# Kernel optimization log

Hardware: AMD Instinct MI355X
Metric: run time of the kernel (lower is better)

Reference implementation:

```python
import jax, jax.numpy as jnp
import numpy as np

BATCH, NODES, HIDDEN = 64, 207, 64
DT = 0.01
STEPS = 100  # integrate t from 0 to 1 with Euler-Maruyama


def _gcn(y3, A, W, b):
    # y3: [B, N, H] -> tanh(A @ Y @ W + b)
    return jnp.tanh(jnp.einsum('mn,bnh->bmh', A, y3) @ W + b)


def setup_inputs() -> dict:
    key = jax.random.key(0)
    ks = jax.random.split(key, 8)
    scale = 1.0 / np.sqrt(HIDDEN)
    x = jax.random.normal(ks[0], (BATCH, NODES, HIDDEN), dtype=jnp.float32)
    A = jax.random.uniform(ks[1], (NODES, NODES), dtype=jnp.float32)
    A = A / A.sum(axis=-1, keepdims=True)  # row-normalized adjacency
    W_trend = scale * jax.random.normal(ks[2], (HIDDEN, HIDDEN), dtype=jnp.float32)
    b_trend = jnp.zeros((HIDDEN,), dtype=jnp.float32)
    W_diff = scale * jax.random.normal(ks[3], (HIDDEN, HIDDEN), dtype=jnp.float32)
    b_diff = jnp.zeros((HIDDEN,), dtype=jnp.float32)
    W_out = scale * jax.random.normal(ks[4], (HIDDEN, HIDDEN * HIDDEN), dtype=jnp.float32)
    b_out = jnp.zeros((HIDDEN * HIDDEN,), dtype=jnp.float32)
    return {"x": x, "A": A, "W_trend": W_trend, "b_trend": b_trend,
            "W_diff": W_diff, "b_diff": b_diff, "W_out": W_out, "b_out": b_out}


def reference(x, A, W_trend, b_trend, W_diff, b_diff, W_out, b_out):
    B = x.shape[0]
    y0 = x.reshape(B, -1)  # [B, N*H]
    noise_keys = jax.random.split(jax.random.key(42), STEPS)
    sqrt_dt = jnp.sqrt(jnp.asarray(DT, dtype=y0.dtype))
    dt = jnp.asarray(DT, dtype=y0.dtype)

    def step(y, k):
        y3 = y.reshape(B, NODES, HIDDEN)
        # Abstract_SDE scales both drift and diffusion by 0.1
        F = 0.1 * _gcn(y3, A, W_trend, b_trend).reshape(B, -1)
        G = 0.1 * _gcn(y3, A, W_diff, b_diff).reshape(B, -1)
        dW = sqrt_dt * jax.random.normal(k, y.shape, dtype=y.dtype)
        return y + F * dt + G * dW, None

    yT, _ = jax.lax.scan(step, y0, noise_keys)
    z = yT.reshape(B, NODES, HIDDEN)
    z = z @ W_out + b_out  # [B, N, H*H]
    return jnp.tanh(z.reshape(B, NODES, HIDDEN, HIDDEN))
```

## Files before the change

kernel.cpp:

```cpp
#include <hip/hip_runtime.h>
#include <cstdint>

#define BATCH 64
#define NODES 207
#define HID   64
#define NH    (NODES*HID)
#define TOT   (BATCH*NH)
#define NSTEPS 100
#define MT 28
#define NT 8
#define ASTR 208

__device__ __forceinline__ uint32_t rotl32(uint32_t v, int n) {
    return (v << n) | (v >> (32 - n));
}

__device__ __forceinline__ void threefry2x32(uint32_t k0, uint32_t k1,
                                             uint32_t& x0, uint32_t& x1) {
    uint32_t ks0 = k0, ks1 = k1, ks2 = k0 ^ k1 ^ 0x1BD11BDAu;
    x0 += ks0; x1 += ks1;
#define TF_ROUND(r) { x0 += x1; x1 = rotl32(x1, (r)); x1 ^= x0; }
    TF_ROUND(13) TF_ROUND(15) TF_ROUND(26) TF_ROUND(6)
    x0 += ks1; x1 += ks2 + 1u;
    TF_ROUND(17) TF_ROUND(29) TF_ROUND(16) TF_ROUND(24)
    x0 += ks2; x1 += ks0 + 2u;
    TF_ROUND(13) TF_ROUND(15) TF_ROUND(26) TF_ROUND(6)
    x0 += ks0; x1 += ks1 + 3u;
    TF_ROUND(17) TF_ROUND(29) TF_ROUND(16) TF_ROUND(24)
    x0 += ks1; x1 += ks2 + 4u;
    TF_ROUND(13) TF_ROUND(15) TF_ROUND(26) TF_ROUND(6)
    x0 += ks2; x1 += ks0 + 5u;
#undef TF_ROUND
}

__device__ __forceinline__ float erfinv32(float x) {
    float w = -log1pf(-x * x);
    float p;
    if (w < 5.0f) {
        w = w - 2.5f;
        p =             2.81022636e-08f;
        p = fmaf(p, w,  3.43273939e-07f);
        p = fmaf(p, w, -3.5233877e-06f);
        p = fmaf(p, w, -4.39150654e-06f);
        p = fmaf(p, w,  0.00021858087f);
        p = fmaf(p, w, -0.00125372503f);
        p = fmaf(p, w, -0.00417768164f);
        p = fmaf(p, w,  0.246640727f);
        p = fmaf(p, w,  1.50140941f);
    } else {
        w = sqrtf(w) - 3.0f;
        p =            -0.000200214257f;
        p = fmaf(p, w,  0.000100950558f);
        p = fmaf(p, w,  0.00134934322f);
        p = fmaf(p, w, -0.00367342844f);
        p = fmaf(p, w,  0.00573950773f);
        p = fmaf(p, w, -0.0076224613f);
        p = fmaf(p, w,  0.00943887047f);
        p = fmaf(p, w,  1.00167406f);
        p = fmaf(p, w,  2.83297682f);
    }
    return p * x;
}

__device__ __forceinline__ float bits_to_normal(uint32_t bits) {
    uint32_t fb = (bits >> 9) | 0x3f800000u;
    float f = __uint_as_float(fb) - 1.0f;
    const float lo = -0.99999994f;
    float u = f * 2.0f + lo;
    u = fmaxf(lo, u);
    return 1.41421356237f * erfinv32(u);
}


__global__ void k_init(const float* __restrict__ x, float* __restrict__ y,
                       uint32_t* __restrict__ keys) {
    int tid = blockIdx.x * blockDim.x + threadIdx.x;
    int n4 = TOT / 4;
    int stride = gridDim.x * blockDim.x;
    for (int i = tid; i < n4; i += stride) {
        ((float4*)y)[i] = ((const float4*)x)[i];
    }
    if (tid < NSTEPS) {
        uint32_t x0 = 0u, x1 = (uint32_t)tid;
        threefry2x32(0u, 42u, x0, x1);
        keys[2*tid]   = x0;
        keys[2*tid+1] = x1;
    }
}

__global__ __launch_bounds__(512) void k_fused(const float* __restrict__ A,
                                               const float* __restrict__ yin,
                                               float* __restrict__ yout,
                                               const float* __restrict__ Wt,
                                               const float* __restrict__ bt,
                                               const float* __restrict__ Wd,
                                               const float* __restrict__ bd,
                                               const uint32_t* __restrict__ keys,
                                               int s) {
    __shared__ __align__(16) float Alds[MT * ASTR];
    __shared__ __align__(16) float AYs[MT * HID];
    int b  = blockIdx.x;
    int m0 = blockIdx.y * MT;
    int h  = threadIdx.x & 63;
    int r  = __builtin_amdgcn_readfirstlane((int)(threadIdx.x >> 6));

    for (int row = r; row < MT; row += 8) {
        int m = m0 + row;
        const float* src = A + (size_t)m * NODES;
        bool v = (m < NODES);
        for (int c = h; c < NODES; c += 64)
            Alds[row*ASTR + c] = v ? src[c] : 0.0f;
    }
    __syncthreads();

    int rl[4];
#pragma unroll
    for (int i = 0; i < 4; ++i) {
        int t = r + 8*i;
        rl[i] = (t < MT) ? t : (MT - 1);
    }

    const float* yb = yin + (size_t)b * NH;
    float acc[4] = {0.f, 0.f, 0.f, 0.f};
#pragma unroll 2
    for (int n = 0; n < 204; n += 4) {
        float y0 = yb[(n+0)*HID + h];
        float y1 = yb[(n+1)*HID + h];
        float y2 = yb[(n+2)*HID + h];
        float y3 = yb[(n+3)*HID + h];
#pragma unroll
        for (int i = 0; i < 4; ++i) {
            float4 a4 = *(const float4*)&Alds[rl[i]*ASTR + n];
            acc[i] = fmaf(a4.x, y0, acc[i]);
            acc[i] = fmaf(a4.y, y1, acc[i]);
            acc[i] = fmaf(a4.z, y2, acc[i]);
            acc[i] = fmaf(a4.w, y3, acc[i]);
        }
    }
#pragma unroll 1
    for (int n = 204; n < NODES; ++n) {
        float yv = yb[n*HID + h];
#pragma unroll
        for (int i = 0; i < 4; ++i)
            acc[i] = fmaf(Alds[rl[i]*ASTR + n], yv, acc[i]);
    }

#pragma unroll
    for (int i = 0; i < 4; ++i) {
        int t = r + 8*i;
        if (t < MT) AYs[t*HID + h] = acc[i];
    }

    float accT[4] = {0.f, 0.f, 0.f, 0.f};
    float accD[4] = {0.f, 0.f, 0.f, 0.f};
#pragma unroll 2
    for (int k = 0; k < HID; k += 4) {
        float wt0 = Wt[(k+0)*HID + h], wt1 = Wt[(k+1)*HID + h];
        float wt2 = Wt[(k+2)*HID + h], wt3 = Wt[(k+3)*HID + h];
        float wd0 = Wd[(k+0)*HID + h], wd1 = Wd[(k+1)*HID + h];
        float wd2 = Wd[(k+2)*HID + h], wd3 = Wd[(k+3)*HID + h];
#pragma unroll
        for (int i = 0; i < 4; ++i) {
            float4 a4 = *(const float4*)&AYs[rl[i]*HID + k];
            accT[i] = fmaf(a4.x, wt0, accT[i]);
            accT[i] = fmaf(a4.y, wt1, accT[i]);
            accT[i] = fmaf(a4.z, wt2, accT[i]);
            accT[i] = fmaf(a4.w, wt3, accT[i]);
            accD[i] = fmaf(a4.x, wd0, accD[i]);
            accD[i] = fmaf(a4.y, wd1, accD[i]);
            accD[i] = fmaf(a4.z, wd2, accD[i]);
            accD[i] = fmaf(a4.w, wd3, accD[i]);
        }
    }

    uint32_t kk0 = keys[2*s], kk1 = keys[2*s+1];
    float btv = bt[h], bdv = bd[h];
#pragma unroll
    for (int i = 0; i < 4; ++i) {
        int t = r + 8*i;
        int m = m0 + t;
        if (t < MT && m < NODES) {
            float F = 0.1f * tanhf(accT[i] + btv);
            float G = 0.1f * tanhf(accD[i] + bdv);
            uint32_t j = (uint32_t)(((size_t)b*NODES + m)*HID + h);
            uint32_t x0 = 0u, x1 = j;
            threefry2x32(kk0, kk1, x0, x1);
            float nrm = bits_to_normal(x0 ^ x1);
            float dW  = 0.1f * nrm;
            float yold = yb[(size_t)m*HID + h];
            yout[(size_t)b*NH + (size_t)m*HID + h] = (yold + F * 0.01f) + G * dW;
        }
    }
}

#define OR 16
__global__ __launch_bounds__(256) void k_out(const float* __restrict__ y,
                                             const float* __restrict__ Wo,
                                             const float* __restrict__ bo,
                                             float* __restrict__ out) {
    int r0   = blockIdx.x * OR;
    int col0 = blockIdx.y * 1024 + threadIdx.x * 4;
    const float* yb = y + (size_t)r0 * HID;
    float4 acc[OR];
#pragma unroll
    for (int r = 0; r < OR; ++r) acc[r] = make_float4(0.f, 0.f, 0.f, 0.f);
#pragma unroll 4
    for (int k = 0; k < HID; ++k) {
        float4 wv = *(const float4*)&Wo[(size_t)k*4096 + col0];
#pragma unroll
        for (int r = 0; r < OR; ++r) {
            float yv = yb[r*HID + k];
            acc[r].x = fmaf(yv, wv.x, acc[r].x);
            acc[r].y = fmaf(yv, wv.y, acc[r].y);
            acc[r].z = fmaf(yv, wv.z, acc[r].z);
            acc[r].w = fmaf(yv, wv.w, acc[r].w);
        }
    }
    float4 bb = *(const float4*)&bo[col0];
#pragma unroll
    for (int r = 0; r < OR; ++r) {
        float4 o;
        o.x = tanhf(acc[r].x + bb.x);
        o.y = tanhf(acc[r].y + bb.y);
        o.z = tanhf(acc[r].z + bb.z);
        o.w = tanhf(acc[r].w + bb.w);
        *(float4*)&out[(size_t)(r0 + r)*4096 + col0] = o;
    }
}

extern "C" void kernel_launch(void* const* d_in, const int* in_sizes, int n_in,
                              void* d_out, int out_size, void* d_ws, size_t ws_size,
                              hipStream_t stream) {
    const float* x  = (const float*)d_in[0];
    const float* A  = (const float*)d_in[1];
    const float* Wt = (const float*)d_in[2];
    const float* bt = (const float*)d_in[3];
    const float* Wd = (const float*)d_in[4];
    const float* bd = (const float*)d_in[5];
    const float* Wo = (const float*)d_in[6];
    const float* bo = (const float*)d_in[7];
    float* out = (float*)d_out;

    float* y0 = (float*)d_ws;
    float* y1 = y0 + TOT;
    uint32_t* keys = (uint32_t*)(y1 + TOT);

    k_init<<<512, 256, 0, stream>>>(x, y0, keys);
    float* cur = y0;
    float* nxt = y1;
    for (int s = 0; s < NSTEPS; ++s) {
        k_fused<<<dim3(BATCH, NT), 512, 0, stream>>>(A, cur, nxt, Wt, bt, Wd, bd, keys, s);
        float* t = cur; cur = nxt; nxt = t;
    }
    k_out<<<dim3(NH/OR, 4096/1024), 256, 0, stream>>>(cur, Wo, bo, out);
}
```

Measured before the change: 2.707 ms.

## Replace per-step launches with persistent kernel using per-batch global barriers

The 100 per-step kernel launches become one persistent kernel of 512 blocks. Blocks for the same batch sync through a per-batch atomic counter barrier, and the A tile stays in LDS across all steps. The step keys are now computed per block in LDS. This removes launch overhead and the repeated A reload, but it depends on all 512 blocks being co-resident (launch_bounds 512,2) and adds spin-wait cost at every step. After 100 steps the final state lands in y0, which is what k_out reads.

After: 5.764 ms. 2.13x slower.

```diff
diff --git a/kernel.cpp b/kernel.cpp
--- a/kernel.cpp
+++ b/kernel.cpp
@@ -73,36 +73,33 @@
 
 
 __global__ void k_init(const float* __restrict__ x, float* __restrict__ y,
-                       uint32_t* __restrict__ keys) {
+                       uint32_t* __restrict__ bar) {
     int tid = blockIdx.x * blockDim.x + threadIdx.x;
     int n4 = TOT / 4;
     int stride = gridDim.x * blockDim.x;
     for (int i = tid; i < n4; i += stride) {
         ((float4*)y)[i] = ((const float4*)x)[i];
     }
-    if (tid < NSTEPS) {
-        uint32_t x0 = 0u, x1 = (uint32_t)tid;
-        threefry2x32(0u, 42u, x0, x1);
-        keys[2*tid]   = x0;
-        keys[2*tid+1] = x1;
-    }
-}
-
-__global__ __launch_bounds__(512) void k_fused(const float* __restrict__ A,
-                                               const float* __restrict__ yin,
-                                               float* __restrict__ yout,
-                                               const float* __restrict__ Wt,
-                                               const float* __restrict__ bt,
-                                               const float* __restrict__ Wd,
-                                               const float* __restrict__ bd,
-                                               const uint32_t* __restrict__ keys,
-                                               int s) {
+    if (tid < 1024) bar[tid] = 0u;
+}
+
+__global__ __launch_bounds__(512, 2) void k_persist(const float* __restrict__ A,
+                                                    float* y0g,
+                                                    float* y1g,
+                                                    const float* __restrict__ Wt,
+                                                    const float* __restrict__ bt,
+                                                    const float* __restrict__ Wd,
+                                                    const float* __restrict__ bd,
+                                                    uint32_t* bar) {
     __shared__ __align__(16) float Alds[MT * ASTR];
     __shared__ __align__(16) float AYs[MT * HID];
-    int b  = blockIdx.x;
-    int m0 = blockIdx.y * MT;
-    int h  = threadIdx.x & 63;
-    int r  = __builtin_amdgcn_readfirstlane((int)(threadIdx.x >> 6));
+    __shared__ uint32_t Klds[2 * NSTEPS];
+    int bid = blockIdx.x;
+    int b   = bid >> 3;
+    int t8  = bid & 7;
+    int m0  = t8 * MT;
+    int h   = threadIdx.x & 63;
+    int r   = __builtin_amdgcn_readfirstlane((int)(threadIdx.x >> 6));
 
     for (int row = r; row < MT; row += 8) {
         int m = m0 + row;
@@ -111,6 +108,12 @@
         for (int c = h; c < NODES; c += 64)
             Alds[row*ASTR + c] = v ? src[c] : 0.0f;
     }
+    if (threadIdx.x < NSTEPS) {
+        uint32_t x0 = 0u, x1 = (uint32_t)threadIdx.x;
+        threefry2x32(0u, 42u, x0, x1);
+        Klds[2*threadIdx.x]   = x0;
+        Klds[2*threadIdx.x+1] = x1;
+    }
     __syncthreads();
 
     int rl[4];
@@ -120,76 +123,99 @@
         rl[i] = (t < MT) ? t : (MT - 1);
     }
 
-    const float* yb = yin + (size_t)b * NH;
-    float acc[4] = {0.f, 0.f, 0.f, 0.f};
+    float* cur = y0g;
+    float* nxt = y1g;
+    uint32_t* mybar = bar + b * 16;
+
+#pragma unroll 1
+    for (int s = 0; s < NSTEPS; ++s) {
+        const float* yb = cur + (size_t)b * NH;
+
+        float acc[4] = {0.f, 0.f, 0.f, 0.f};
 #pragma unroll 2
-    for (int n = 0; n < 204; n += 4) {
-        float y0 = yb[(n+0)*HID + h];
-        float y1 = yb[(n+1)*HID + h];
-        float y2 = yb[(n+2)*HID + h];
-        float y3 = yb[(n+3)*HID + h];
+        for (int n = 0; n < 204; n += 4) {
+            float y0 = yb[(n+0)*HID + h];
+            float y1 = yb[(n+1)*HID + h];
+            float y2 = yb[(n+2)*HID + h];
+            float y3 = yb[(n+3)*HID + h];
+#pragma unroll
+            for (int i = 0; i < 4; ++i) {
+                float4 a4 = *(const float4*)&Alds[rl[i]*ASTR + n];
+                acc[i] = fmaf(a4.x, y0, acc[i]);
+                acc[i] = fmaf(a4.y, y1, acc[i]);
+                acc[i] = fmaf(a4.z, y2, acc[i]);
+                acc[i] = fmaf(a4.w, y3, acc[i]);
+            }
+        }
+#pragma unroll 1
+        for (int n = 204; n < NODES; ++n) {
+            float yv = yb[n*HID + h];
+#pragma unroll
+            for (int i = 0; i < 4; ++i)
+                acc[i] = fmaf(Alds[rl[i]*ASTR + n], yv, acc[i]);
+        }
+
 #pragma unroll
         for (int i = 0; i < 4; ++i) {
-            float4 a4 = *(const float4*)&Alds[rl[i]*ASTR + n];
-            acc[i] = fmaf(a4.x, y0, acc[i]);
-            acc[i] = fmaf(a4.y, y1, acc[i]);
-            acc[i] = fmaf(a4.z, y2, acc[i]);
-            acc[i] = fmaf(a4.w, y3, acc[i]);
-        }
-    }
-#pragma unroll 1
-    for (int n = 204; n < NODES; ++n) {
-        float yv = yb[n*HID + h];
-#pragma unroll
-        for (int i = 0; i < 4; ++i)
-            acc[i] = fmaf(Alds[rl[i]*ASTR + n], yv, acc[i]);
-    }
-
-#pragma unroll
-    for (int i = 0; i < 4; ++i) {
-        int t = r + 8*i;
-        if (t < MT) AYs[t*HID + h] = acc[i];
-    }
-
-    float accT[4] = {0.f, 0.f, 0.f, 0.f};
-    float accD[4] = {0.f, 0.f, 0.f, 0.f};
+            int t = r + 8*i;
+            if (t < MT) AYs[t*HID + h] = acc[i];
+        }
+
+        float accT[4] = {0.f, 0.f, 0.f, 0.f};
+        float accD[4] = {0.f, 0.f, 0.f, 0.f};
 #pragma unroll 2
-    for (int k = 0; k < HID; k += 4) {
-        float wt0 = Wt[(k+0)*HID + h], wt1 = Wt[(k+1)*HID + h];
-        float wt2 = Wt[(k+2)*HID + h], wt3 = Wt[(k+3)*HID + h];
-        float wd0 = Wd[(k+0)*HID + h], wd1 = Wd[(k+1)*HID + h];
-        float wd2 = Wd[(k+2)*HID + h], wd3 = Wd[(k+3)*HID + h];
+        for (int k = 0; k < HID; k += 4) {
+            float wt0 = Wt[(k+0)*HID + h], wt1 = Wt[(k+1)*HID + h];
+            float wt2 = Wt[(k+2)*HID + h], wt3 = Wt[(k+3)*HID + h];
+            float wd0 = Wd[(k+0)*HID + h], wd1 = Wd[(k+1)*HID + h];
+            float wd2 = Wd[(k+2)*HID + h], wd3 = Wd[(k+3)*HID + h];
+#pragma unroll
+            for (int i = 0; i < 4; ++i) {
+                float4 a4 = *(const float4*)&AYs[rl[i]*HID + k];
+                accT[i] = fmaf(a4.x, wt0, accT[i]);
+                accT[i] = fmaf(a4.y, wt1, accT[i]);
+                accT[i] = fmaf(a4.z, wt2, accT[i]);
+                accT[i] = fmaf(a4.w, wt3, accT[i]);
+                accD[i] = fmaf(a4.x, wd0, accD[i]);
+                accD[i] = fmaf(a4.y, wd1, accD[i]);
+                accD[i] = fmaf(a4.z, wd2, accD[i]);
+                accD[i] = fmaf(a4.w, wd3, accD[i]);
+            }
+        }
+
+        uint32_t kk0 = Klds[2*s], kk1 = Klds[2*s+1];
+        float btv = bt[h], bdv = bd[h];
 #pragma unroll
         for (int i = 0; i < 4; ++i) {
-            float4 a4 = *(const float4*)&AYs[rl[i]*HID + k];
-            accT[i] = fmaf(a4.x, wt0, accT[i]);
-            accT[i] = fmaf(a4.y, wt1, accT[i]);
-            accT[i] = fmaf(a4.z, wt2, accT[i]);
-            accT[i] = fmaf(a4.w, wt3, accT[i]);
-            accD[i] = fmaf(a4.x, wd0, accD[i]);
-            accD[i] = fmaf(a4.y, wd1, accD[i]);
-            accD[i] = fmaf(a4.z, wd2, accD[i]);
-            accD[i] = fmaf(a4.w, wd3, accD[i]);
-        }
-    }
-
-    uint32_t kk0 = keys[2*s], kk1 = keys[2*s+1];
-    float btv = bt[h], bdv = bd[h];
-#pragma unroll
-    for (int i = 0; i < 4; ++i) {
-        int t = r + 8*i;
-        int m = m0 + t;
-        if (t < MT && m < NODES) {
-            float F = 0.1f * tanhf(accT[i] + btv);
-            float G = 0.1f * tanhf(accD[i] + bdv);
-            uint32_t j = (uint32_t)(((size_t)b*NODES + m)*HID + h);
-            uint32_t x0 = 0u, x1 = j;
-            threefry2x32(kk0, kk1, x0, x1);
-            float nrm = bits_to_normal(x0 ^ x1);
-            float dW  = 0.1f * nrm;
-            float yold = yb[(size_t)m*HID + h];
-            yout[(size_t)b*NH + (size_t)m*HID + h] = (yold + F * 0.01f) + G * dW;
-        }
+            int t = r + 8*i;
+            int m = m0 + t;
+            if (t < MT && m < NODES) {
+                float F = 0.1f * tanhf(accT[i] + btv);
+                float G = 0.1f * tanhf(accD[i] + bdv);
+                uint32_t j = (uint32_t)(((size_t)b*NODES + m)*HID + h);
+                uint32_t x0 = 0u, x1 = j;
+                threefry2x32(kk0, kk1, x0, x1);
+                float nrm = bits_to_normal(x0 ^ x1);
+                float dW  = 0.1f * nrm;
+                float yold = yb[(size_t)m*HID + h];
+                nxt[(size_t)b*NH + (size_t)m*HID + h] = (yold + F * 0.01f) + G * dW;
+            }
+        }
+
+        __syncthreads();
+        if (threadIdx.x == 0) {
+            __threadfence();
+            atomicAdd(mybar, 1u);
+            uint32_t tgt = 8u * (uint32_t)(s + 1);
+            while (__hip_atomic_load(mybar, __ATOMIC_ACQUIRE,
+                                     __HIP_MEMORY_SCOPE_AGENT) < tgt) {
+                __builtin_amdgcn_s_sleep(8);
+            }
+            __threadfence();
+        }
+        __syncthreads();
+
+        float* tmp = cur; cur = nxt; nxt = tmp;
     }
 }
 
@@ -243,14 +269,9 @@
 
     float* y0 = (float*)d_ws;
     float* y1 = y0 + TOT;
-    uint32_t* keys = (uint32_t*)(y1 + TOT);
-
-    k_init<<<512, 256, 0, stream>>>(x, y0, keys);
-    float* cur = y0;
-    float* nxt = y1;
-    for (int s = 0; s < NSTEPS; ++s) {
-        k_fused<<<dim3(BATCH, NT), 512, 0, stream>>>(A, cur, nxt, Wt, bt, Wd, bd, keys, s);
-        float* t = cur; cur = nxt; nxt = t;
-    }
-    k_out<<<dim3(NH/OR, 4096/1024), 256, 0, stream>>>(cur, Wo, bo, out);
-}
+    uint32_t* bar = (uint32_t*)(y1 + TOT);
+
+    k_init<<<512, 256, 0, stream>>>(x, y0, bar);
+    k_persist<<<512, 512, 0, stream>>>(A, y0, y1, Wt, bt, Wd, bd, bar);
+    k_out<<<dim3(NH/OR, 4096/1024), 256, 0, stream>>>(y0, Wo, bo, out);
+}
```

## Stage Y slice in LDS transposed and read padded A from global

Applied to the files above, without the earlier changes.

Swaps which operand sits in shared memory for the A·Y product. The per-batch Y slice is now loaded once into LDS, transposed per hidden column with float4 packing. A is pre-padded to a 208 stride in the init kernel and read from global/cache as float4 with wave-uniform addresses. The previous version re-read Y from global in the inner loop and loaded A tiles into LDS. This also lets the Euler update read the old y from LDS. The cost is larger LDS per block, which may lower occupancy. The strided float4 LDS reads by h may also cause bank conflicts.

Result: no change. 2.669 ms (-1.4%).

```diff
diff --git a/kernel.cpp b/kernel.cpp
--- a/kernel.cpp
+++ b/kernel.cpp
@@ -9,7 +9,9 @@
 #define NSTEPS 100
 #define MT 28
 #define NT 8
-#define ASTR 208
+#define APSTR 208
+#define YSTR 212
+#define YQ   53
 
 __device__ __forceinline__ uint32_t rotl32(uint32_t v, int n) {
     return (v << n) | (v >> (32 - n));
@@ -72,13 +74,18 @@
 }
 
 
-__global__ void k_init(const float* __restrict__ x, float* __restrict__ y,
+__global__ void k_init(const float* __restrict__ x, const float* __restrict__ A,
+                       float* __restrict__ y, float* __restrict__ A_pad,
                        uint32_t* __restrict__ keys) {
     int tid = blockIdx.x * blockDim.x + threadIdx.x;
-    int n4 = TOT / 4;
     int stride = gridDim.x * blockDim.x;
-    for (int i = tid; i < n4; i += stride) {
+    for (int i = tid; i < TOT/4; i += stride) {
         ((float4*)y)[i] = ((const float4*)x)[i];
+    }
+    for (int i = tid; i < NODES*APSTR; i += stride) {
+        int row = i / APSTR;
+        int col = i - row*APSTR;
+        A_pad[i] = (col < NODES) ? A[row*NODES + col] : 0.0f;
     }
     if (tid < NSTEPS) {
         uint32_t x0 = 0u, x1 = (uint32_t)tid;
@@ -88,7 +95,7 @@
     }
 }
 
-__global__ __launch_bounds__(512) void k_fused(const float* __restrict__ A,
+__global__ __launch_bounds__(512) void k_fused(const float* __restrict__ A_pad,
                                                const float* __restrict__ yin,
                                                float* __restrict__ yout,
                                                const float* __restrict__ Wt,
@@ -97,52 +104,63 @@
                                                const float* __restrict__ bd,
                                                const uint32_t* __restrict__ keys,
                                                int s) {
-    __shared__ __align__(16) float Alds[MT * ASTR];
+    __shared__ __align__(16) float Ylds[64 * YSTR];
     __shared__ __align__(16) float AYs[MT * HID];
     int b  = blockIdx.x;
     int m0 = blockIdx.y * MT;
     int h  = threadIdx.x & 63;
     int r  = __builtin_amdgcn_readfirstlane((int)(threadIdx.x >> 6));
 
-    for (int row = r; row < MT; row += 8) {
-        int m = m0 + row;
-        const float* src = A + (size_t)m * NODES;
-        bool v = (m < NODES);
-        for (int c = h; c < NODES; c += 64)
-            Alds[row*ASTR + c] = v ? src[c] : 0.0f;
+    const float* yb = yin + (size_t)b * NH;
+
+    {
+        int g0 = (int)(threadIdx.x >> 6);
+#pragma unroll
+        for (int it = 0; it < 7; ++it) {
+            int g = g0 + (it << 3);
+            if (g < YQ) {
+                int n = g << 2;
+                float4 v;
+                v.x = (n+0 < NODES) ? yb[(n+0)*HID + h] : 0.0f;
+                v.y = (n+1 < NODES) ? yb[(n+1)*HID + h] : 0.0f;
+                v.z = (n+2 < NODES) ? yb[(n+2)*HID + h] : 0.0f;
+                v.w = (n+3 < NODES) ? yb[(n+3)*HID + h] : 0.0f;
+                ((float4*)Ylds)[h*YQ + g] = v;
+            }
+        }
     }
     __syncthreads();
 
     int rl[4];
+    const float* Ap[4];
 #pragma unroll
     for (int i = 0; i < 4; ++i) {
         int t = r + 8*i;
         rl[i] = (t < MT) ? t : (MT - 1);
-    }
-
-    const float* yb = yin + (size_t)b * NH;
+        int m = m0 + rl[i];
+        int mc = (m < NODES) ? m : (NODES - 1);
+        Ap[i] = A_pad + (size_t)mc * APSTR;
+    }
+
     float acc[4] = {0.f, 0.f, 0.f, 0.f};
 #pragma unroll 2
     for (int n = 0; n < 204; n += 4) {
-        float y0 = yb[(n+0)*HID + h];
-        float y1 = yb[(n+1)*HID + h];
-        float y2 = yb[(n+2)*HID + h];
-        float y3 = yb[(n+3)*HID + h];
+        float4 y4 = ((const float4*)Ylds)[h*YQ + (n >> 2)];
 #pragma unroll
         for (int i = 0; i < 4; ++i) {
-            float4 a4 = *(const float4*)&Alds[rl[i]*ASTR + n];
-            acc[i] = fmaf(a4.x, y0, acc[i]);
-            acc[i] = fmaf(a4.y, y1, acc[i]);
-            acc[i] = fmaf(a4.z, y2, acc[i]);
-            acc[i] = fmaf(a4.w, y3, acc[i]);
+            float4 a4 = *(const float4*)&Ap[i][n];
+            acc[i] = fmaf(a4.x, y4.x, acc[i]);
+            acc[i] = fmaf(a4.y, y4.y, acc[i]);
+            acc[i] = fmaf(a4.z, y4.z, acc[i]);
+            acc[i] = fmaf(a4.w, y4.w, acc[i]);
         }
     }
 #pragma unroll 1
     for (int n = 204; n < NODES; ++n) {
-        float yv = yb[n*HID + h];
+        float yv = Ylds[h*YSTR + n];
 #pragma unroll
         for (int i = 0; i < 4; ++i)
-            acc[i] = fmaf(Alds[rl[i]*ASTR + n], yv, acc[i]);
+            acc[i] = fmaf(Ap[i][n], yv, acc[i]);
     }
 
 #pragma unroll
@@ -187,7 +205,7 @@
             threefry2x32(kk0, kk1, x0, x1);
             float nrm = bits_to_normal(x0 ^ x1);
             float dW  = 0.1f * nrm;
-            float yold = yb[(size_t)m*HID + h];
+            float yold = Ylds[h*YSTR + m];
             yout[(size_t)b*NH + (size_t)m*HID + h] = (yold + F * 0.01f) + G * dW;
         }
     }
@@ -244,12 +262,13 @@
     float* y0 = (float*)d_ws;
     float* y1 = y0 + TOT;
     uint32_t* keys = (uint32_t*)(y1 + TOT);
-
-    k_init<<<512, 256, 0, stream>>>(x, y0, keys);
+    float* A_pad = (float*)(keys + 256);
+
+    k_init<<<512, 256, 0, stream>>>(x, A, y0, A_pad, keys);
     float* cur = y0;
     float* nxt = y1;
     for (int s = 0; s < NSTEPS; ++s) {
-        k_fused<<<dim3(BATCH, NT), 512, 0, stream>>>(A, cur, nxt, Wt, bt, Wd, bd, keys, s);
+        k_fused<<<dim3(BATCH, NT), 512, 0, stream>>>(A_pad, cur, nxt, Wt, bt, Wd, bd, keys, s);
         float* t = cur; cur = nxt; nxt = t;
     }
     k_out<<<dim3(NH/OR, 4096/1024), 256, 0, stream>>>(cur, Wo, bo, out);
```
